# Kernel tuning notes

Hardware: AMD Instinct MI355X
Metric: run time of the kernel (lower is better)

Reference implementation:

```python
import jax, jax.numpy as jnp
import numpy as np

N, E, G = 10000, 50000, 500
MAX_Z = 64
C0, C1, C2 = 128, 64, 32            # multiplicities of l=0,1,2 irreps ('128x0e+64x1e+32x2e')
D = C0 + 3 * C1 + 5 * C2            # 480 total feature dim
H = 4                               # num_heads
HC0, HC1, HC2 = C0 // H, C1 // H, C2 // H   # irreps_head '32x0e+16x1o+8x2e'
HD = HC0 + 3 * HC1 + 5 * HC2        # 120 head dim
NB = 128                            # number_of_basis
CUTOFF = 5.0                        # max_radius
T_DEQ = 2                           # DEQ fixed-point iterations (unrolled)
NDEQ, NBLK = 5, 6                   # num_layers=6: 5 DEQ blocks + 1 decoder block
NW = C0 + 2 * C1 + 2 * C2           # 320 radial modulation weights per message
AVG_DEGREE = 16.0
AVG_NUM_NODES = 21.0
FDIM = 512                          # irreps_feature '512x0e'


def split(x):
    n = x.shape[0]
    return x[:, :C0], x[:, C0:C0 + 3 * C1].reshape(n, C1, 3), x[:, C0 + 3 * C1:].reshape(n, C2, 5)


def merge(s, v1, v2):
    n = s.shape[0]
    return jnp.concatenate([s, v1.reshape(n, -1), v2.reshape(n, -1)], axis=-1)


def eq_layernorm(x, eps=1e-5):
    # EquivariantLayerNormV2: center l=0, RMS-normalize each l-block per node
    s, v1, v2 = split(x)
    s = s - s.mean(-1, keepdims=True)
    s = s * jax.lax.rsqrt((s * s).mean(-1, keepdims=True) + eps)
    v1 = v1 * jax.lax.rsqrt((v1 * v1).sum(-1).mean(-1) + eps)[:, None, None]
    v2 = v2 * jax.lax.rsqrt((v2 * v2).sum(-1).mean(-1) + eps)[:, None, None]
    return merge(s, v1, v2)


def eq_linear(x, W0, W1, W2):
    # e3nn Linear: block-diagonal per irrep degree, mixes channels only
    s, v1, v2 = split(x)
    return merge(s @ W0, jnp.einsum('ncm,cd->ndm', v1, W1), jnp.einsum('ncm,cd->ndm', v2, W2))


def sph_harm(u):
    # real spherical harmonics lmax=2, component normalization
    x, y, z = u[:, 0], u[:, 1], u[:, 2]
    y1 = jnp.sqrt(3.0) * u
    y2 = jnp.stack([jnp.sqrt(15.0) * x * y, jnp.sqrt(15.0) * y * z,
                    jnp.sqrt(1.25) * (3.0 * z * z - 1.0),
                    jnp.sqrt(15.0) * x * z, jnp.sqrt(3.75) * (x * x - y * y)], -1)
    return y1, y2


def radial(rbf, R1, R2, R3):
    # fc_neurons [128,64,64] radial MLP -> per-path tensor-product weights
    return jax.nn.silu(jax.nn.silu(rbf @ R1) @ R2) @ R3


def modulate(s_e, v1_e, v2_e, y1, y2, P1, P2, w):
    # depthwise tensor product x_src (x) Y(sh), radial-weighted paths:
    # 0x0->0, 1x0->1, 0x1->1, 2x0->2, 0x2->2
    w0, w1, w2, w3, w4 = jnp.split(w, [C0, C0 + C1, C0 + 2 * C1, C0 + 2 * C1 + C2], -1)
    m_s = s_e * w0
    m_v1 = v1_e * w1[:, :, None] + (s_e @ P1)[:, :, None] * y1[:, None, :] * w2[:, :, None]
    m_v2 = v2_e * w3[:, :, None] + (s_e @ P2)[:, :, None] * y2[:, None, :] * w4[:, :, None]
    return m_s, m_v1, m_v2


def to_heads(s, v1, v2):
    n = s.shape[0]
    return jnp.concatenate([s.reshape(n, H, HC0), v1.reshape(n, H, HC1 * 3), v2.reshape(n, H, HC2 * 5)], -1)


def from_heads(a):
    n = a.shape[0]
    return merge(a[:, :, :HC0].reshape(n, C0),
                 a[:, :, HC0:HC0 + 3 * HC1].reshape(n, C1, 3),
                 a[:, :, HC0 + 3 * HC1:].reshape(n, C2, 5))


def block(x, src, dst, rbf, y1, y2, i, Wq0, Wq1, Wq2, P1, P2, R1, R2, R3, Wp0, Wp1, Wp2, Wg, Wi0, Wi1, Wi2, Wo0, Wo1, Wo2):
    # LN -> dot-product graph attention -> LN -> gated equivariant FFN, both residual
    n = x.shape[0]
    xn = eq_layernorm(x)
    q = to_heads(*split(eq_linear(xn, Wq0[i], Wq1[i], Wq2[i])))      # [N,H,HD]
    w = radial(rbf, R1[i], R2[i], R3[i])                             # [E,2*NW]
    s, v1, v2 = split(xn)
    s_e, v1_e, v2_e = s[src], v1[src], v2[src]
    k = to_heads(*modulate(s_e, v1_e, v2_e, y1, y2, P1[i], P2[i], w[:, :NW]))
    v = to_heads(*modulate(s_e, v1_e, v2_e, y1, y2, P1[i], P2[i], w[:, NW:]))
    logits = (q[dst] * k).sum(-1) / jnp.sqrt(jnp.float32(HD))        # [E,H] invariant
    m = jax.ops.segment_max(logits, dst, num_segments=n)
    e = jnp.exp(logits - m[dst])
    denom = jax.ops.segment_sum(e, dst, num_segments=n)
    alpha = e / (denom[dst] + 1e-9)
    att = jax.ops.segment_sum(alpha[:, :, None] * v, dst, num_segments=n)  # [N,H,HD]
    x = x + eq_linear(from_heads(att), Wp0[i], Wp1[i], Wp2[i])
    xn2 = eq_layernorm(x)
    y = eq_linear(xn2, Wi0[i], Wi1[i], Wi2[i])
    ys, yv1, yv2 = split(y)
    g = jax.nn.sigmoid(xn2[:, :C0] @ Wg[i])                          # gates for l>0
    y = merge(jax.nn.silu(ys), yv1 * g[:, :C1, None], yv2 * g[:, C1:, None])
    return x + eq_linear(y, Wo0[i], Wo1[i], Wo2[i])


def setup_inputs() -> dict:
    key = jax.random.key(0)
    ks = iter(jax.random.split(key, 64))
    f32 = jnp.float32
    pos = jax.random.normal(next(ks), (N, 3), f32) * 2.0
    atom_z = jax.random.randint(next(ks), (N,), 0, MAX_Z)
    edge_src = jax.random.randint(next(ks), (E,), 0, N)
    edge_dst = jax.random.randint(next(ks), (E,), 0, N)
    batch_seg = jnp.sort(jax.random.randint(next(ks), (N,), 0, G))
    def W(shape, fan):
        return jax.random.normal(next(ks), shape, f32) / np.sqrt(fan).astype(np.float32)
    inp = dict(pos=pos, atom_z=atom_z, edge_src=edge_src, edge_dst=edge_dst, batch_seg=batch_seg)
    inp.update(
        atom_table=W((MAX_Z, C0), 1.0),
        Pd1=W((C0, C1), C0), Pd2=W((C0, C2), C0),
        Rd1=W((NB, 64), NB), Rd2=W((64, 64), 64), Rd3=W((64, NW), 64),
        Wq0=W((NBLK, C0, C0), C0), Wq1=W((NBLK, C1, C1), C1), Wq2=W((NBLK, C2, C2), C2),
        P1=W((NBLK, C0, C1), C0), P2=W((NBLK, C0, C2), C0),
        R1=W((NBLK, NB, 64), NB), R2=W((NBLK, 64, 64), 64), R3=W((NBLK, 64, 2 * NW), 64),
        Wp0=W((NBLK, C0, C0), C0), Wp1=W((NBLK, C1, C1), C1), Wp2=W((NBLK, C2, C2), C2),
        Wg=W((NBLK, C0, C1 + C2), C0),
        Wi0=W((NBLK, C0, C0), C0), Wi1=W((NBLK, C1, C1), C1), Wi2=W((NBLK, C2, C2), C2),
        Wo0=W((NBLK, C0, C0), C0), Wo1=W((NBLK, C1, C1), C1), Wo2=W((NBLK, C2, C2), C2),
        Wf=W((C0, FDIM), C0), Wh1=W((FDIM, FDIM), FDIM), Wh2=W((FDIM, 1), FDIM),
    )
    return inp


def reference(pos, atom_z, edge_src, edge_dst, batch_seg, atom_table, Pd1, Pd2, Rd1, Rd2, Rd3, Wq0, Wq1, Wq2, P1, P2, R1, R2, R3, Wp0, Wp1, Wp2, Wg, Wi0, Wi1, Wi2, Wo0, Wo1, Wo2, Wf, Wh1, Wh2):
    vec = pos[edge_dst] - pos[edge_src]
    r = jnp.sqrt((vec * vec).sum(-1) + 1e-12)
    u = vec / r[:, None]
    mus = jnp.linspace(0.0, CUTOFF, NB, dtype=pos.dtype)
    sigma = CUTOFF / NB
    rbf = jnp.exp(-0.5 * ((r[:, None] - mus) / sigma) ** 2)          # gaussian RBF [E,NB]
    y1, y2 = sph_harm(u)
    # atom embedding (scalars only) + edge-degree embedding
    s_atom = jax.nn.one_hot(atom_z, MAX_Z, dtype=pos.dtype) @ atom_table
    wd = radial(rbf, Rd1, Rd2, Rd3)
    z1 = jnp.zeros((E, C1, 3), pos.dtype)
    z2 = jnp.zeros((E, C2, 5), pos.dtype)
    m_s, m_v1, m_v2 = modulate(s_atom[edge_src], z1, z2, y1, y2, Pd1, Pd2, wd)
    deg = merge(jax.ops.segment_sum(m_s, edge_dst, num_segments=N),
                jax.ops.segment_sum(m_v1, edge_dst, num_segments=N),
                jax.ops.segment_sum(m_v2, edge_dst, num_segments=N)) / jnp.sqrt(jnp.float32(AVG_DEGREE))
    inj = merge(s_atom, jnp.zeros((N, C1, 3), pos.dtype), jnp.zeros((N, C2, 5), pos.dtype)) + deg
    bp = (Wq0, Wq1, Wq2, P1, P2, R1, R2, R3, Wp0, Wp1, Wp2, Wg, Wi0, Wi1, Wi2, Wo0, Wo1, Wo2)
    # DEQ fixed-point iterations over the 5 implicit blocks, with input injection
    z = jnp.zeros((N, D), pos.dtype)
    for _ in range(T_DEQ):
        x = z + inj
        for i in range(NDEQ):
            x = block(x, edge_src, edge_dst, rbf, y1, y2, i, *bp)
        z = x
    x = block(z, edge_src, edge_dst, rbf, y1, y2, NBLK - 1, *bp)     # decoder block
    feat = split(x)[0] @ Wf                                          # 512x0e invariant features
    feat = feat - feat.mean(-1, keepdims=True)
    feat = feat * jax.lax.rsqrt((feat * feat).mean(-1, keepdims=True) + 1e-5)
    e_node = jax.nn.silu(feat @ Wh1) @ Wh2                           # per-node energy [N,1]
    return jax.ops.segment_sum(e_node, batch_seg, num_segments=G) / jnp.sqrt(jnp.float32(AVG_NUM_NODES))
```

## Files before the change

### kernel.cpp

```cpp
#include <hip/hip_runtime.h>
#include <hip/hip_bf16.h>
#include <math.h>

#define NN 10000
#define NE 50000
#define NBLK 6
#define MAXD 256
#define V1_OFF (NN*128)
#define V2_OFF (NN*320)

typedef __hip_bfloat16 bf16;
typedef __attribute__((ext_vector_type(8))) short short8;
typedef __attribute__((ext_vector_type(4))) float f32x4;

__device__ __forceinline__ float ldw(const float* p){ return *p; }
__device__ __forceinline__ float ldw(const bf16* p){ return __bfloat162float(*p); }
__device__ __forceinline__ void stw(float* p, float v){ *p = v; }
__device__ __forceinline__ void stw(bf16* p, float v){ *p = __float2bfloat16(v); }

template<typename OutT>
__global__ __launch_bounds__(256)
void mgemm_kernel(const bf16* __restrict__ A, const bf16* __restrict__ Bt,
                  OutT* __restrict__ C, int M, int Nn, int K,
                  int lda, int ldc, int epi)
{
  __shared__ __align__(16) unsigned short Ash[64][40];
  __shared__ __align__(16) unsigned short Bsh[64][40];
  int tid  = threadIdx.x;
  int wid  = tid >> 6, lane = tid & 63;
  int wr   = wid >> 1, wc = wid & 1;
  int rowBase = blockIdx.x * 64, colBase = blockIdx.y * 64;
  int fr = lane & 15;
  int fk = (lane >> 4) * 8;
  f32x4 acc[2][2] = {};
  int am = tid >> 2, ako = (tid & 3) * 8;

  for (int k0 = 0; k0 < K; k0 += 32) {
    {
      int gm = rowBase + am;
      short8 v = {0,0,0,0,0,0,0,0};
      if (gm < M) v = *reinterpret_cast<const short8*>(A + (long)gm * lda + k0 + ako);
      *reinterpret_cast<short8*>(&Ash[am][ako]) = v;
    }
    {
      int gn = colBase + am;
      short8 v = {0,0,0,0,0,0,0,0};
      if (gn < Nn) v = *reinterpret_cast<const short8*>(Bt + (long)gn * K + k0 + ako);
      *reinterpret_cast<short8*>(&Bsh[am][ako]) = v;
    }
    __syncthreads();
    short8 a0 = *reinterpret_cast<const short8*>(&Ash[wr*32 +      fr][fk]);
    short8 a1 = *reinterpret_cast<const short8*>(&Ash[wr*32 + 16 + fr][fk]);
    short8 b0 = *reinterpret_cast<const short8*>(&Bsh[wc*32 +      fr][fk]);
    short8 b1 = *reinterpret_cast<const short8*>(&Bsh[wc*32 + 16 + fr][fk]);
    acc[0][0] = __builtin_amdgcn_mfma_f32_16x16x32_bf16(a0, b0, acc[0][0], 0, 0, 0);
    acc[0][1] = __builtin_amdgcn_mfma_f32_16x16x32_bf16(a0, b1, acc[0][1], 0, 0, 0);
    acc[1][0] = __builtin_amdgcn_mfma_f32_16x16x32_bf16(a1, b0, acc[1][0], 0, 0, 0);
    acc[1][1] = __builtin_amdgcn_mfma_f32_16x16x32_bf16(a1, b1, acc[1][1], 0, 0, 0);
    __syncthreads();
  }
  int erow = (lane >> 4) * 4, ecol = lane & 15;
  #pragma unroll
  for (int tm = 0; tm < 2; tm++) {
    #pragma unroll
    for (int tn = 0; tn < 2; tn++) {
      #pragma unroll
      for (int r = 0; r < 4; r++) {
        int gm = rowBase + wr*32 + tm*16 + erow + r;
        int gn = colBase + wc*32 + tn*16 + ecol;
        if (gm < M && gn < Nn) {
          float v = acc[tm][tn][r];
          long off = (long)gm * ldc + gn;
          if (epi == 1)      v = v / (1.f + expf(-v));
          else if (epi == 2) v = v + ldw(&C[off]);
          else if (epi == 3) v = 1.f / (1.f + expf(-v));
          stw(&C[off], v);
        }
      }
    }
  }
}

struct GSeg {
  const bf16* A; const bf16* Bt; char* C;
  int M, N, K, lda, ldc, epi, outBf16, blk0, nbx;
};

__global__ __launch_bounds__(256)
void gseg_kernel(GSeg s0, GSeg s1, GSeg s2, GSeg s3, int nseg)
{
  GSeg s = s0;
  int b = blockIdx.x;
  if (nseg > 1 && b >= s1.blk0) s = s1;
  if (nseg > 2 && b >= s2.blk0) s = s2;
  if (nseg > 3 && b >= s3.blk0) s = s3;
  int rel = b - s.blk0;
  int bx = rel % s.nbx, by = rel / s.nbx;

  __shared__ __align__(16) unsigned short Ash[64][40];
  __shared__ __align__(16) unsigned short Bsh[64][40];
  int tid  = threadIdx.x;
  int wid  = tid >> 6, lane = tid & 63;
  int wr   = wid >> 1, wc = wid & 1;
  int rowBase = bx * 64, colBase = by * 64;
  int fr = lane & 15;
  int fk = (lane >> 4) * 8;
  f32x4 acc[2][2] = {};
  int am = tid >> 2, ako = (tid & 3) * 8;

  for (int k0 = 0; k0 < s.K; k0 += 32) {
    {
      int gm = rowBase + am;
      short8 v = {0,0,0,0,0,0,0,0};
      if (gm < s.M) v = *reinterpret_cast<const short8*>(s.A + (long)gm * s.lda + k0 + ako);
      *reinterpret_cast<short8*>(&Ash[am][ako]) = v;
    }
    {
      int gn = colBase + am;
      short8 v = {0,0,0,0,0,0,0,0};
      if (gn < s.N) v = *reinterpret_cast<const short8*>(s.Bt + (long)gn * s.K + k0 + ako);
      *reinterpret_cast<short8*>(&Bsh[am][ako]) = v;
    }
    __syncthreads();
    short8 a0 = *reinterpret_cast<const short8*>(&Ash[wr*32 +      fr][fk]);
    short8 a1 = *reinterpret_cast<const short8*>(&Ash[wr*32 + 16 + fr][fk]);
    short8 b0 = *reinterpret_cast<const short8*>(&Bsh[wc*32 +      fr][fk]);
    short8 b1 = *reinterpret_cast<const short8*>(&Bsh[wc*32 + 16 + fr][fk]);
    acc[0][0] = __builtin_amdgcn_mfma_f32_16x16x32_bf16(a0, b0, acc[0][0], 0, 0, 0);
    acc[0][1] = __builtin_amdgcn_mfma_f32_16x16x32_bf16(a0, b1, acc[0][1], 0, 0, 0);
    acc[1][0] = __builtin_amdgcn_mfma_f32_16x16x32_bf16(a1, b0, acc[1][0], 0, 0, 0);
    acc[1][1] = __builtin_amdgcn_mfma_f32_16x16x32_bf16(a1, b1, acc[1][1], 0, 0, 0);
    __syncthreads();
  }
  int erow = (lane >> 4) * 4, ecol = lane & 15;
  #pragma unroll
  for (int tm = 0; tm < 2; tm++) {
    #pragma unroll
    for (int tn = 0; tn < 2; tn++) {
      #pragma unroll
      for (int r = 0; r < 4; r++) {
        int gm = rowBase + wr*32 + tm*16 + erow + r;
        int gn = colBase + wc*32 + tn*16 + ecol;
        if (gm < s.M && gn < s.N) {
          float v = acc[tm][tn][r];
          long off = (long)gm * s.ldc + gn;
          if (s.epi == 1)      v = v / (1.f + expf(-v));
          else if (s.epi == 2) v = v + (s.outBf16 ? ldw((const bf16*)s.C + off)
                                                 : ldw((const float*)s.C + off));
          else if (s.epi == 3) v = 1.f / (1.f + expf(-v));
          if (s.outBf16) stw((bf16*)s.C + off, v);
          else           stw((float*)s.C + off, v);
        }
      }
    }
  }
}

__global__ void transp_kernel(const float* __restrict__ src, bf16* __restrict__ dst,
                              int R, int C, long sSrc, long sDst)
{
  src += (long)blockIdx.z * sSrc;
  dst += (long)blockIdx.z * sDst;
  int idx = blockIdx.x * 256 + threadIdx.x;
  if (idx < R * C) {
    int r = idx / C, c = idx - r * C;
    dst[(long)c * R + r] = __float2bfloat16(src[idx]);
  }
}

__global__ void gather_atom_kernel(const int* __restrict__ z, const float* __restrict__ tab,
                                   float* __restrict__ s_atom, bf16* __restrict__ s_atom_bf)
{
  int idx = blockIdx.x * 256 + threadIdx.x;
  if (idx < NN * 128) {
    int n = idx >> 7, c = idx & 127;
    float v = tab[z[n] * 128 + c];
    s_atom[idx] = v;
    s_atom_bf[idx] = __float2bfloat16(v);
  }
}

__global__ void hist_kernel(const int* __restrict__ dst, int* __restrict__ counts)
{
  int e = blockIdx.x * 256 + threadIdx.x;
  if (e < NE) atomicAdd(&counts[dst[e]], 1);
}

__global__ __launch_bounds__(1024)
void scan_kernel(const int* __restrict__ counts, int* __restrict__ indptr,
                 int* __restrict__ nextp)
{
  __shared__ int totals[1024];
  const int PER = (NN + 1023) / 1024;
  int tid = threadIdx.x;
  int base = tid * PER;
  int local[PER];
  int s = 0;
  #pragma unroll
  for (int i = 0; i < PER; i++) {
    int idx = base + i;
    int c = (idx < NN) ? counts[idx] : 0;
    local[i] = s; s += c;
  }
  totals[tid] = s;
  __syncthreads();
  for (int off = 1; off < 1024; off <<= 1) {
    int v = (tid >= off) ? totals[tid - off] : 0;
    __syncthreads();
    totals[tid] += v;
    __syncthreads();
  }
  int prefix = (tid > 0) ? totals[tid - 1] : 0;
  #pragma unroll
  for (int i = 0; i < PER; i++) {
    int idx = base + i;
    if (idx < NN) { indptr[idx] = prefix + local[i]; nextp[idx] = prefix + local[i]; }
  }
  if (tid == 1023) indptr[NN] = totals[1023];
}

__global__ void scatter_kernel(const int* __restrict__ dst, int* __restrict__ nextp,
                               int* __restrict__ order)
{
  int e = blockIdx.x * 256 + threadIdx.x;
  if (e < NE) {
    int p = atomicAdd(&nextp[dst[e]], 1);
    order[p] = e;
  }
}

__global__ void dhist_kernel(const int* __restrict__ indptr, int* __restrict__ bins)
{
  int n = blockIdx.x * 256 + threadIdx.x;
  if (n < NN) {
    int d = indptr[n+1] - indptr[n]; if (d > MAXD-1) d = MAXD-1;
    atomicAdd(&bins[MAXD-1-d], 1);
  }
}
__global__ __launch_bounds__(256)
void dscan_kernel(const int* __restrict__ bins, int* __restrict__ boff)
{
  __shared__ int tmp[MAXD];
  int t = threadIdx.x;
  tmp[t] = bins[t];
  __syncthreads();
  for (int off = 1; off < MAXD; off <<= 1) {
    int v = (t >= off) ? tmp[t-off] : 0;
    __syncthreads();
    tmp[t] += v;
    __syncthreads();
  }
  boff[t] = tmp[t] - bins[t];
}
__global__ void dplace_kernel(const int* __restrict__ indptr, int* __restrict__ boff,
                              int* __restrict__ norder)
{
  int n = blockIdx.x * 256 + threadIdx.x;
  if (n < NN) {
    int d = indptr[n+1] - indptr[n]; if (d > MAXD-1) d = MAXD-1;
    int pos = atomicAdd(&boff[MAXD-1-d], 1);
    norder[pos] = n;
  }
}

__global__ __launch_bounds__(128)
void edge_perm_kernel(const float* __restrict__ pos, const int* __restrict__ esrc,
                      const int* __restrict__ edst, const int* __restrict__ order,
                      int* __restrict__ srcp, bf16* __restrict__ rbf,
                      float* __restrict__ y1, float* __restrict__ y2)
{
  int idx = blockIdx.x, t = threadIdx.x;
  int e = order[idx];
  int s = esrc[e], d = edst[e];
  float vx = pos[d*3+0] - pos[s*3+0];
  float vy = pos[d*3+1] - pos[s*3+1];
  float vz = pos[d*3+2] - pos[s*3+2];
  float r = sqrtf(vx*vx + vy*vy + vz*vz + 1e-12f);
  float mu = t * (5.0f / 127.0f);
  const float inv_sig = 128.0f / 5.0f;
  float zq = (r - mu) * inv_sig;
  rbf[(long)idx * 128 + t] = __float2bfloat16(expf(-0.5f * zq * zq));
  if (t == 0) {
    srcp[idx] = s;
    float inv = 1.f / r;
    float ux = vx*inv, uy = vy*inv, uz = vz*inv;
    const float s3  = 1.7320508075688772f;
    const float s15 = 3.872983346207417f;
    y1[idx*3+0] = s3*ux; y1[idx*3+1] = s3*uy; y1[idx*3+2] = s3*uz;
    y2[idx*5+0] = s15*ux*uy;
    y2[idx*5+1] = s15*uy*uz;
    y2[idx*5+2] = 1.118033988749895f * (3.f*uz*uz - 1.f);
    y2[idx*5+3] = s15*ux*uz;
    y2[idx*5+4] = 1.9364916731037085f * (ux*ux - uy*uy);
  }
}

__global__ void copy_kernel(const float* __restrict__ a, float* __restrict__ b, int n)
{
  int i = blockIdx.x * 256 + threadIdx.x;
  if (i < n) b[i] = a[i];
}

__global__ void addinj_kernel(float* __restrict__ x, const float* __restrict__ inj, int n)
{
  int i = blockIdx.x * 256 + threadIdx.x;
  if (i < n) x[i] += inj[i];
}

__global__ void cvt128_kernel(const float* __restrict__ a, bf16* __restrict__ b)
{
  int i = blockIdx.x * 256 + threadIdx.x;
  if (i < NN * 128) b[i] = __float2bfloat16(a[i]);
}

__global__ __launch_bounds__(64)
void ln_kernel(const float* __restrict__ x, bf16* __restrict__ ob)
{
  int n = blockIdx.x, t = threadIdx.x;
  bool lo = t < 32;
  int t32 = t & 31;
  float s0 = x[n*128 + t], s1 = x[n*128 + 64 + t];
  float v1v[3], v2v[5];
  #pragma unroll
  for (int m = 0; m < 3; m++) v1v[m] = x[V1_OFF + m*NN*64 + n*64 + t];
  #pragma unroll
  for (int m = 0; m < 5; m++) v2v[m] = lo ? x[V2_OFF + m*NN*32 + n*32 + t32] : 0.f;
  float ssum = s0 + s1, ssq = s0*s0 + s1*s1;
  float q1 = v1v[0]*v1v[0] + v1v[1]*v1v[1] + v1v[2]*v1v[2];
  float q2 = 0.f;
  #pragma unroll
  for (int m = 0; m < 5; m++) q2 += v2v[m]*v2v[m];
  #pragma unroll
  for (int d = 32; d >= 1; d >>= 1) {
    ssum += __shfl_xor(ssum, d);
    ssq  += __shfl_xor(ssq, d);
    q1   += __shfl_xor(q1, d);
    q2   += __shfl_xor(q2, d);
  }
  float mu  = ssum * (1.f/128.f);
  float var = fmaxf(ssq * (1.f/128.f) - mu*mu, 0.f);
  float is  = rsqrtf(var + 1e-5f);
  float i1  = rsqrtf(q1 * (1.f/64.f) + 1e-5f);
  float i2  = rsqrtf(q2 * (1.f/32.f) + 1e-5f);
  ob[n*128 + t]      = __float2bfloat16((s0 - mu) * is);
  ob[n*128 + 64 + t] = __float2bfloat16((s1 - mu) * is);
  #pragma unroll
  for (int m = 0; m < 3; m++)
    ob[V1_OFF + m*NN*64 + n*64 + t] = __float2bfloat16(v1v[m] * i1);
  if (lo) {
    #pragma unroll
    for (int m = 0; m < 5; m++)
      ob[V2_OFF + m*NN*32 + n*32 + t32] = __float2bfloat16(v2v[m] * i2);
  }
}

__global__ __launch_bounds__(64)
void deg_inj_kernel(const int* __restrict__ indptr, const int* __restrict__ srcp,
                    const bf16* __restrict__ wd,
                    const float* __restrict__ s_atom, const float* __restrict__ spd1,
                    const float* __restrict__ spd2, const float* __restrict__ y1,
                    const float* __restrict__ y2, float* __restrict__ inj)
{
  int n = blockIdx.x, t = threadIdx.x;
  bool lo = t < 32;
  int t32 = t & 31;
  float acc0 = 0, acc1 = 0, a1[3] = {0,0,0}, a2[5] = {0,0,0,0,0};
  int beg = indptr[n], end = indptr[n+1];
  for (int idx = beg; idx < end; ++idx) {
    int s = srcp[idx];
    const bf16* we = wd + (size_t)idx * 320;
    acc0 += s_atom[s*128 + t]      * ldw(&we[t]);
    acc1 += s_atom[s*128 + 64 + t] * ldw(&we[64 + t]);
    float sp1e = spd1[s*64 + t];
    float w2k = ldw(&we[192 + t]);
    #pragma unroll
    for (int m = 0; m < 3; m++) a1[m] += sp1e * y1[idx*3+m] * w2k;
    float sp2e = lo ? spd2[s*32 + t32] : 0.f;
    float w4k  = lo ? ldw(&we[288 + t32]) : 0.f;
    #pragma unroll
    for (int m = 0; m < 5; m++) a2[m] += sp2e * y2[idx*5+m] * w4k;
  }
  const float inv = 0.25f;
  inj[n*128 + t]      = s_atom[n*128 + t]      + acc0 * inv;
  inj[n*128 + 64 + t] = s_atom[n*128 + 64 + t] + acc1 * inv;
  #pragma unroll
  for (int m = 0; m < 3; m++) inj[V1_OFF + m*NN*64 + n*64 + t] = a1[m] * inv;
  if (lo) {
    #pragma unroll
    for (int m = 0; m < 5; m++) inj[V2_OFF + m*NN*32 + n*32 + t32] = a2[m] * inv;
  }
}

__global__ __launch_bounds__(64)
void attn_kernel(const int* __restrict__ norder,
                 const int* __restrict__ indptr, const int* __restrict__ srcp,
                 const bf16* __restrict__ w,
                 const bf16* __restrict__ xn, const bf16* __restrict__ qcat,
                 const bf16* __restrict__ qv1b, const bf16* __restrict__ qv2b,
                 const float* __restrict__ y1, const float* __restrict__ y2,
                 bf16* __restrict__ att)
{
  int n = norder[blockIdx.x];
  int t = threadIdx.x;
  bool lo = t < 32;
  int t32 = t & 31;
  const float qscl = 0.09128709291752769f;
  float qs0 = ldw(&qcat[n*224 + t]) * qscl, qs1 = ldw(&qcat[n*224 + 64 + t]) * qscl;
  float qv1[3], qv2[5];
  #pragma unroll
  for (int m = 0; m < 3; m++) qv1[m] = ldw(&qv1b[m*NN*64 + n*64 + t]) * qscl;
  #pragma unroll
  for (int m = 0; m < 5; m++) qv2[m] = lo ? ldw(&qv2b[m*NN*32 + n*32 + t32]) * qscl : 0.f;
  const int h_s0 = t >> 5, h_s1 = 2 + (t >> 5), h_v1 = t >> 4, h_v2 = t32 >> 3;
  float m_run[4] = {-1e30f, -1e30f, -1e30f, -1e30f};
  float d_run[4] = {0, 0, 0, 0};
  float as0 = 0, as1 = 0, av1[3] = {0,0,0}, av2[5] = {0,0,0,0,0};
  int beg = indptr[n], end = indptr[n+1];
  for (int idx = beg; idx < end; ++idx) {
    int s = srcp[idx];
    const bf16* we = w + (size_t)idx * 640;
    float sE0 = ldw(&xn[s*128 + t]), sE1 = ldw(&xn[s*128 + 64 + t]);
    float v1E[3];
    #pragma unroll
    for (int m = 0; m < 3; m++) v1E[m] = ldw(&xn[V1_OFF + m*NN*64 + s*64 + t]);
    float v2E[5];
    #pragma unroll
    for (int m = 0; m < 5; m++) v2E[m] = lo ? ldw(&xn[V2_OFF + m*NN*32 + s*32 + t32]) : 0.f;
    float sp1e = ldw(&qcat[s*224 + 128 + t]);
    float sp2e = lo ? ldw(&qcat[s*224 + 192 + t32]) : 0.f;
    float Y1[3], Y2[5];
    #pragma unroll
    for (int m = 0; m < 3; m++) Y1[m] = y1[idx*3+m];
    #pragma unroll
    for (int m = 0; m < 5; m++) Y2[m] = lo ? y2[idx*5+m] : 0.f;
    float part[4] = {0,0,0,0};
    part[h_s0] += qs0 * (sE0 * ldw(&we[t]));
    part[h_s1] += qs1 * (sE1 * ldw(&we[64 + t]));
    float w1k = ldw(&we[128 + t]), w2k = ldw(&we[192 + t]);
    #pragma unroll
    for (int m = 0; m < 3; m++) part[h_v1] += qv1[m] * (v1E[m]*w1k + sp1e*Y1[m]*w2k);
    float w3k = lo ? ldw(&we[256 + t32]) : 0.f, w4k = lo ? ldw(&we[288 + t32]) : 0.f;
    #pragma unroll
    for (int m = 0; m < 5; m++) part[h_v2] += qv2[m] * (v2E[m]*w3k + sp2e*Y2[m]*w4k);
    #pragma unroll
    for (int d = 1; d < 64; d <<= 1) {
      #pragma unroll
      for (int h = 0; h < 4; h++) part[h] += __shfl_xor(part[h], d);
    }
    float scl[4], pp[4];
    #pragma unroll
    for (int h = 0; h < 4; h++) {
      float logit = part[h];
      float nm = fmaxf(m_run[h], logit);
      scl[h] = expf(m_run[h] - nm);
      pp[h]  = expf(logit - nm);
      d_run[h] = d_run[h] * scl[h] + pp[h];
      m_run[h] = nm;
    }
    as0 = as0 * scl[h_s0] + pp[h_s0] * (sE0 * ldw(&we[320 + t]));
    as1 = as1 * scl[h_s1] + pp[h_s1] * (sE1 * ldw(&we[384 + t]));
    float w1v = ldw(&we[448 + t]), w2v = ldw(&we[512 + t]);
    #pragma unroll
    for (int m = 0; m < 3; m++)
      av1[m] = av1[m] * scl[h_v1] + pp[h_v1] * (v1E[m]*w1v + sp1e*Y1[m]*w2v);
    float w3v = lo ? ldw(&we[576 + t32]) : 0.f, w4v = lo ? ldw(&we[608 + t32]) : 0.f;
    #pragma unroll
    for (int m = 0; m < 5; m++)
      av2[m] = av2[m] * scl[h_v2] + pp[h_v2] * (v2E[m]*w3v + sp2e*Y2[m]*w4v);
  }
  float r0 = 1.f / (d_run[h_s0] + 1e-9f);
  float r1 = 1.f / (d_run[h_s1] + 1e-9f);
  att[n*128 + t]      = __float2bfloat16(as0 * r0);
  att[n*128 + 64 + t] = __float2bfloat16(as1 * r1);
  float rv1 = 1.f / (d_run[h_v1] + 1e-9f);
  #pragma unroll
  for (int m = 0; m < 3; m++)
    att[V1_OFF + m*NN*64 + n*64 + t] = __float2bfloat16(av1[m] * rv1);
  if (lo) {
    float rv2 = 1.f / (d_run[h_v2] + 1e-9f);
    #pragma unroll
    for (int m = 0; m < 5; m++)
      att[V2_OFF + m*NN*32 + n*32 + t32] = __float2bfloat16(av2[m] * rv2);
  }
}

__global__ void gate_kernel(const bf16* __restrict__ ycat, bf16* __restrict__ ybs,
                            bf16* __restrict__ yv1, bf16* __restrict__ yv2)
{
  int idx = blockIdx.x * 256 + threadIdx.x;
  if (idx >= NN * 480) return;
  if (idx < NN * 128) {
    int n = idx >> 7, c = idx & 127;
    float v = ldw(&ycat[n*224 + c]);
    ybs[idx] = __float2bfloat16(v / (1.f + expf(-v)));
  } else if (idx < NN * 320) {
    int rel = idx - NN * 128;
    int n = (rel % (NN * 64)) / 64;
    int c = rel % 64;
    float g = ldw(&ycat[n*224 + 128 + c]);
    g = 1.f / (1.f + expf(-g));
    yv1[rel] = __float2bfloat16(__bfloat162float(yv1[rel]) * g);
  } else {
    int rel = idx - NN * 320;
    int n = (rel % (NN * 32)) / 32;
    int c = rel % 32;
    float g = ldw(&ycat[n*224 + 192 + c]);
    g = 1.f / (1.f + expf(-g));
    yv2[rel] = __float2bfloat16(__bfloat162float(yv2[rel]) * g);
  }
}

__global__ __launch_bounds__(64)
void ln512_kernel(float* __restrict__ f, bf16* __restrict__ fb)
{
  int n = blockIdx.x, t = threadIdx.x;
  float v[8];
  float s = 0, sq = 0;
  #pragma unroll
  for (int i = 0; i < 8; i++) {
    v[i] = f[(long)n*512 + i*64 + t];
    s += v[i]; sq += v[i]*v[i];
  }
  #pragma unroll
  for (int d = 32; d >= 1; d >>= 1) { s += __shfl_xor(s, d); sq += __shfl_xor(sq, d); }
  float mu  = s * (1.f/512.f);
  float var = fmaxf(sq * (1.f/512.f) - mu*mu, 0.f);
  float inv = rsqrtf(var + 1e-5f);
  #pragma unroll
  for (int i = 0; i < 8; i++) {
    float o = (v[i] - mu) * inv;
    fb[(long)n*512 + i*64 + t] = __float2bfloat16(o);
  }
}

__global__ __launch_bounds__(64)
void dot_seg_kernel(const float* __restrict__ h, const float* __restrict__ w2,
                    const int* __restrict__ bseg, float* __restrict__ out)
{
  int n = blockIdx.x, t = threadIdx.x;
  float acc = 0;
  #pragma unroll
  for (int i = 0; i < 8; i++) {
    int j = i*64 + t;
    acc += h[(long)n*512 + j] * w2[j];
  }
  #pragma unroll
  for (int d = 32; d >= 1; d >>= 1) acc += __shfl_xor(acc, d);
  if (t == 0) atomicAdd(&out[bseg[n]], acc * 0.21821789023599236f);
}

extern "C" void kernel_launch(void* const* d_in, const int* in_sizes, int n_in,
                              void* d_out, int out_size, void* d_ws, size_t ws_size,
                              hipStream_t stream)
{
  const float* pos        = (const float*)d_in[0];
  const int*   atom_z     = (const int*)  d_in[1];
  const int*   esrc       = (const int*)  d_in[2];
  const int*   edst       = (const int*)  d_in[3];
  const int*   bseg       = (const int*)  d_in[4];
  const float* atom_table = (const float*)d_in[5];
  const float* Pd1 = (const float*)d_in[6];
  const float* Pd2 = (const float*)d_in[7];
  const float* Rd1 = (const float*)d_in[8];
  const float* Rd2 = (const float*)d_in[9];
  const float* Rd3 = (const float*)d_in[10];
  const float* Wq0 = (const float*)d_in[11];
  const float* Wq1 = (const float*)d_in[12];
  const float* Wq2 = (const float*)d_in[13];
  const float* P1  = (const float*)d_in[14];
  const float* P2  = (const float*)d_in[15];
  const float* R1  = (const float*)d_in[16];
  const float* R2  = (const float*)d_in[17];
  const float* R3  = (const float*)d_in[18];
  const float* Wp0 = (const float*)d_in[19];
  const float* Wp1 = (const float*)d_in[20];
  const float* Wp2 = (const float*)d_in[21];
  const float* Wg  = (const float*)d_in[22];
  const float* Wi0 = (const float*)d_in[23];
  const float* Wi1 = (const float*)d_in[24];
  const float* Wi2 = (const float*)d_in[25];
  const float* Wo0 = (const float*)d_in[26];
  const float* Wo1 = (const float*)d_in[27];
  const float* Wo2 = (const float*)d_in[28];
  const float* Wf  = (const float*)d_in[29];
  const float* Wh1 = (const float*)d_in[30];
  const float* Wh2 = (const float*)d_in[31];
  (void)in_sizes; (void)n_in;

  char* p = (char*)d_ws;
  auto allocB = [&](size_t bytes) -> void* {
    void* r = (void*)p;
    p += (bytes + 255) & ~(size_t)255;
    return r;
  };
  auto allocF = [&](size_t nf) -> float* { return (float*)allocB(nf * 4); };
  auto allocH = [&](size_t nh) -> bf16*  { return (bf16*)allocB(nh * 2); };

  bf16*  rbf   = allocH((size_t)NE * 128);
  float* y1    = allocF((size_t)NE * 3);
  float* y2    = allocF((size_t)NE * 5);
  bf16*  h1    = allocH((size_t)NE * 64);
  bf16*  h2c   = allocH((size_t)6 * NE * 64);
  float* s_at  = allocF((size_t)NN * 128);
  bf16*  s_atb = allocH((size_t)NN * 128);
  float* inj   = allocF((size_t)NN * 480);
  float* x     = allocF((size_t)NN * 480);
  bf16*  xnb   = allocH((size_t)NN * 480);
  bf16*  qcat  = allocH((size_t)NN * 224);
  bf16*  qv1   = allocH((size_t)NN * 192);
  bf16*  qv2   = allocH((size_t)NN * 160);
  bf16*  attb  = allocH((size_t)NN * 480);
  bf16*  ybs   = allocH((size_t)NN * 128);
  int* counts  = (int*)allocB((size_t)NN * 4);
  int* indptr  = (int*)allocB((size_t)(NN + 1) * 4);
  int* nextp   = (int*)allocB((size_t)NN * 4);
  int* order   = (int*)allocB((size_t)NE * 4);
  int* srcp    = (int*)allocB((size_t)NE * 4);
  int* norder  = (int*)allocB((size_t)NN * 4);
  int* dbins   = (int*)allocB((size_t)MAXD * 4);
  int* dboff   = (int*)allocB((size_t)MAXD * 4);
  float* spd1  = allocF((size_t)NN * 64);
  float* spd2  = allocF((size_t)NN * 32);

  bf16*  ycat = qcat;
  bf16*  yv1  = qv1;
  bf16*  yv2  = qv2;
  bf16*  xsb  = s_atb;

  bf16* Pd1t = allocH(64*128);
  bf16* Pd2t = allocH(32*128);
  bf16* Rd1t = allocH(64*128);
  bf16* Rd2t = allocH(64*64);
  bf16* Rd3t = allocH(320*64);
  bf16* catq = allocH((size_t)6*224*128);
  bf16* Wq1t = allocH((size_t)6*64*64);
  bf16* Wq2t = allocH((size_t)6*32*32);
  bf16* R1t  = allocH((size_t)6*64*128);
  bf16* R2t  = allocH((size_t)6*64*64);
  bf16* R3t  = allocH((size_t)6*640*64);
  bf16* Wp0t = allocH((size_t)6*128*128);
  bf16* Wp1t = allocH((size_t)6*64*64);
  bf16* Wp2t = allocH((size_t)6*32*32);
  bf16* cati = allocH((size_t)6*224*128);
  bf16* Wi1t = allocH((size_t)6*64*64);
  bf16* Wi2t = allocH((size_t)6*32*32);
  bf16* Wo0t = allocH((size_t)6*128*128);
  bf16* Wo1t = allocH((size_t)6*64*64);
  bf16* Wo2t = allocH((size_t)6*32*32);
  bf16* Wft  = allocH(512*128);
  bf16* Wh1t = allocH((size_t)512*512);

  size_t used = (size_t)(p - (char*)d_ws);
  size_t avail = (ws_size > used) ? ws_size - used : 0;
  const size_t slotH = (size_t)NE * 640 * sizeof(bf16);

  if (avail < slotH) {
    hipMemsetAsync(d_out, 0, (size_t)out_size * 4, stream);
    return;
  }
  bf16* w = (bf16*)allocB(slotH);

  float* feat  = (float*)w;
  bf16*  featb = (bf16*)(feat + (size_t)NN*512);
  float* hb    = (float*)(featb + (size_t)NN*512);

  auto transp = [&](const float* src, bf16* dst, int R, int C, long sSrc, long sDst, int nz) {
    dim3 g((R*C + 255)/256, 1, nz);
    transp_kernel<<<g, 256, 0, stream>>>(src, dst, R, C, sSrc, sDst);
  };
  auto gemmF = [&](const bf16* A, const bf16* Bt, float* C, int M, int Nn, int K,
                   int lda, int ldc, int epi) {
    dim3 g((M + 63) / 64, (Nn + 63) / 64, 1);
    mgemm_kernel<float><<<g, 256, 0, stream>>>(A, Bt, C, M, Nn, K, lda, ldc, epi);
  };
  auto gemmH = [&](const bf16* A, const bf16* Bt, bf16* C, int M, int Nn, int K,
                   int lda, int ldc, int epi) {
    dim3 g((M + 63) / 64, (Nn + 63) / 64, 1);
    mgemm_kernel<bf16><<<g, 256, 0, stream>>>(A, Bt, C, M, Nn, K, lda, ldc, epi);
  };
  auto mkseg = [&](const bf16* A, const bf16* Bt, void* C, int M, int N, int K,
                   int lda, int ldc, int epi, int outBf16) -> GSeg {
    GSeg g; g.A = A; g.Bt = Bt; g.C = (char*)C; g.M = M; g.N = N; g.K = K;
    g.lda = lda; g.ldc = ldc; g.epi = epi; g.outBf16 = outBf16;
    g.blk0 = 0; g.nbx = (M + 63) / 64;
    return g;
  };
  auto segBlocks = [&](const GSeg& s) -> int { return s.nbx * ((s.N + 63) / 64); };
  auto launch3 = [&](GSeg a, GSeg b, GSeg c) {
    a.blk0 = 0;
    b.blk0 = segBlocks(a);
    c.blk0 = b.blk0 + segBlocks(b);
    int total = c.blk0 + segBlocks(c);
    gseg_kernel<<<total, 256, 0, stream>>>(a, b, c, c, 3);
  };
  auto launch4 = [&](GSeg a, GSeg b, GSeg c, GSeg d) {
    a.blk0 = 0;
    b.blk0 = segBlocks(a);
    c.blk0 = b.blk0 + segBlocks(b);
    d.blk0 = c.blk0 + segBlocks(c);
    int total = d.blk0 + segBlocks(d);
    gseg_kernel<<<total, 256, 0, stream>>>(a, b, c, d, 4);
  };

  transp(Pd1, Pd1t, 128, 64, 0, 0, 1);
  transp(Pd2, Pd2t, 128, 32, 0, 0, 1);
  transp(Rd1, Rd1t, 128, 64, 0, 0, 1);
  transp(Rd2, Rd2t, 64, 64, 0, 0, 1);
  transp(Rd3, Rd3t, 64, 320, 0, 0, 1);
  transp(Wq0, catq,           128, 128, 128*128, 224*128, 6);
  transp(P1,  catq + 128*128, 128, 64,  128*64,  224*128, 6);
  transp(P2,  catq + 192*128, 128, 32,  128*32,  224*128, 6);
  transp(Wq1, Wq1t, 64, 64, 64*64, 64*64, 6);
  transp(Wq2, Wq2t, 32, 32, 32*32, 32*32, 6);
  transp(R1,  R1t, 128, 64, 128*64, 128*64, 6);
  transp(R2,  R2t, 64, 64, 64*64, 64*64, 6);
  transp(R3,  R3t, 64, 640, 64*640, 64*640, 6);
  transp(Wp0, Wp0t, 128, 128, 128*128, 128*128, 6);
  transp(Wp1, Wp1t, 64, 64, 64*64, 64*64, 6);
  transp(Wp2, Wp2t, 32, 32, 32*32, 32*32, 6);
  transp(Wi0, cati,           128, 128, 128*128, 224*128, 6);
  transp(Wg,  cati + 128*128, 128, 96,  128*96,  224*128, 6);
  transp(Wi1, Wi1t, 64, 64, 64*64, 64*64, 6);
  transp(Wi2, Wi2t, 32, 32, 32*32, 32*32, 6);
  transp(Wo0, Wo0t, 128, 128, 128*128, 128*128, 6);
  transp(Wo1, Wo1t, 64, 64, 64*64, 64*64, 6);
  transp(Wo2, Wo2t, 32, 32, 32*32, 32*32, 6);
  transp(Wf,  Wft, 128, 512, 0, 0, 1);
  transp(Wh1, Wh1t, 512, 512, 0, 0, 1);

  hipMemsetAsync(counts, 0, NN * 4, stream);
  hipMemsetAsync(dbins, 0, MAXD * 4, stream);
  hipMemsetAsync(d_out, 0, (size_t)out_size * 4, stream);
  gather_atom_kernel<<<(NN*128 + 255)/256, 256, 0, stream>>>(atom_z, atom_table, s_at, s_atb);
  hist_kernel<<<(NE + 255)/256, 256, 0, stream>>>(edst, counts);
  scan_kernel<<<1, 1024, 0, stream>>>(counts, indptr, nextp);
  scatter_kernel<<<(NE + 255)/256, 256, 0, stream>>>(edst, nextp, order);
  edge_perm_kernel<<<NE, 128, 0, stream>>>(pos, esrc, edst, order, srcp, rbf, y1, y2);
  dhist_kernel<<<(NN + 255)/256, 256, 0, stream>>>(indptr, dbins);
  dscan_kernel<<<1, MAXD, 0, stream>>>(dbins, dboff);
  dplace_kernel<<<(NN + 255)/256, 256, 0, stream>>>(indptr, dboff, norder);
  gemmF(s_atb, Pd1t, spd1, NN, 64, 128, 128, 64, 0);
  gemmF(s_atb, Pd2t, spd2, NN, 32, 128, 128, 32, 0);
  gemmH(rbf, Rd1t, h1, NE, 64, 128, 128, 64, 1);
  gemmH(h1,  Rd2t, h2c, NE, 64, 64, 64, 64, 1);
  gemmH(h2c, Rd3t, w,  NE, 320, 64, 64, 320, 0);
  deg_inj_kernel<<<NN, 64, 0, stream>>>(indptr, srcp, w, s_at, spd1, spd2, y1, y2, inj);
  copy_kernel<<<(NN*480 + 255)/256, 256, 0, stream>>>(inj, x, NN*480);

  for (int i = 0; i < 6; i++) {
    gemmH(rbf, R1t + (size_t)i*64*128, h1, NE, 64, 128, 128, 64, 1);
    gemmH(h1,  R2t + (size_t)i*64*64, h2c + (size_t)i*NE*64, NE, 64, 64, 64, 64, 1);
  }

  auto run_block = [&](int i) {
    const bf16* cq  = catq + (size_t)i * 224 * 128;
    const bf16* q1t = Wq1t + (size_t)i * 64 * 64;
    const bf16* q2t = Wq2t + (size_t)i * 32 * 32;
    const bf16* r3  = R3t  + (size_t)i * 640 * 64;
    const bf16* p0t = Wp0t + (size_t)i * 128 * 128;
    const bf16* p1t = Wp1t + (size_t)i * 64 * 64;
    const bf16* p2t = Wp2t + (size_t)i * 32 * 32;
    const bf16* ci  = cati + (size_t)i * 224 * 128;
    const bf16* i1t = Wi1t + (size_t)i * 64 * 64;
    const bf16* i2t = Wi2t + (size_t)i * 32 * 32;
    const bf16* o0t = Wo0t + (size_t)i * 128 * 128;
    const bf16* o1t = Wo1t + (size_t)i * 64 * 64;
    const bf16* o2t = Wo2t + (size_t)i * 32 * 32;

    ln_kernel<<<NN, 64, 0, stream>>>(x, xnb);
    launch4(mkseg(xnb,          cq,  qcat, NN,   224, 128, 128, 224, 0, 1),
            mkseg(xnb + V1_OFF, q1t, qv1,  3*NN, 64,  64,  64,  64,  0, 1),
            mkseg(xnb + V2_OFF, q2t, qv2,  5*NN, 32,  32,  32,  32,  0, 1),
            mkseg(h2c + (size_t)i*NE*64, r3, w, NE, 640, 64, 64, 640, 0, 1));
    attn_kernel<<<NN, 64, 0, stream>>>(norder, indptr, srcp, w, xnb, qcat, qv1, qv2, y1, y2, attb);
    launch3(mkseg(attb,          p0t, x,          NN,   128, 128, 128, 128, 2, 0),
            mkseg(attb + V1_OFF, p1t, x + V1_OFF, 3*NN, 64,  64,  64,  64,  2, 0),
            mkseg(attb + V2_OFF, p2t, x + V2_OFF, 5*NN, 32,  32,  32,  32,  2, 0));
    ln_kernel<<<NN, 64, 0, stream>>>(x, xnb);
    launch3(mkseg(xnb,          ci,  ycat, NN,   224, 128, 128, 224, 0, 1),
            mkseg(xnb + V1_OFF, i1t, yv1,  3*NN, 64,  64,  64,  64,  0, 1),
            mkseg(xnb + V2_OFF, i2t, yv2,  5*NN, 32,  32,  32,  32,  0, 1));
    gate_kernel<<<(NN*480 + 255)/256, 256, 0, stream>>>(ycat, ybs, yv1, yv2);
    launch3(mkseg(ybs, o0t, x,          NN,   128, 128, 128, 128, 2, 0),
            mkseg(yv1, o1t, x + V1_OFF, 3*NN, 64,  64,  64,  64,  2, 0),
            mkseg(yv2, o2t, x + V2_OFF, 5*NN, 32,  32,  32,  32,  2, 0));
  };

  for (int t = 0; t < 2; t++) {
    if (t == 1) addinj_kernel<<<(NN*480 + 255)/256, 256, 0, stream>>>(x, inj, NN*480);
    for (int i = 0; i < 5; i++) run_block(i);
  }
  run_block(5);

  cvt128_kernel<<<(NN*128 + 255)/256, 256, 0, stream>>>(x, xsb);
  gemmF(xsb, Wft, feat, NN, 512, 128, 128, 512, 0);
  ln512_kernel<<<NN, 64, 0, stream>>>(feat, featb);
  gemmF(featb, Wh1t, hb, NN, 512, 512, 512, 512, 1);
  dot_seg_kernel<<<NN, 64, 0, stream>>>(hb, Wh2, bseg, (float*)d_out);
}
```

Baseline: 2.056 ms.

## Interleave radial weight columns for vector loads and use lazy softmax rescaling

Reorders R3's transposed output columns so each thread's eight per-edge radial weights sit contiguously. The attention kernel can then fetch them with one 16-byte load, plus an 8-byte load for the l=2 lanes, instead of many scalar bf16 loads. The online softmax now rescales only when a logit exceeds the running max by more than 8, and uses fast __expf. This cuts exp calls and multiplies per edge, at the cost of a slightly different numerical path and reliance on the R3 layout matching the edge-weight GEMM output.

```diff
diff --git a/kernel.cpp b/kernel.cpp
--- a/kernel.cpp
+++ b/kernel.cpp
@@ -11,12 +11,17 @@
 
 typedef __hip_bfloat16 bf16;
 typedef __attribute__((ext_vector_type(8))) short short8;
+typedef __attribute__((ext_vector_type(4))) short short4v;
 typedef __attribute__((ext_vector_type(4))) float f32x4;
 
 __device__ __forceinline__ float ldw(const float* p){ return *p; }
 __device__ __forceinline__ float ldw(const bf16* p){ return __bfloat162float(*p); }
 __device__ __forceinline__ void stw(float* p, float v){ *p = v; }
 __device__ __forceinline__ void stw(bf16* p, float v){ *p = __float2bfloat16(v); }
+__device__ __forceinline__ float b2f(short u){
+  unsigned int x = ((unsigned int)(unsigned short)u) << 16;
+  return __builtin_bit_cast(float, x);
+}
 
 template<typename OutT>
 __global__ __launch_bounds__(256)
@@ -168,6 +173,28 @@
   }
 }
 
+__global__ void transp_r3_kernel(const float* __restrict__ src, bf16* __restrict__ dst)
+{
+  int idx = blockIdx.x * 256 + threadIdx.x;
+  if (idx >= NBLK * 640 * 64) return;
+  int blk  = idx / (640 * 64);
+  int rem  = idx - blk * 640 * 64;
+  int newc = rem >> 6;
+  int k    = rem & 63;
+  int oldc;
+  if (newc < 512) {
+    int t = newc >> 3, j = newc & 7;
+    const int base[8] = {0, 64, 128, 192, 320, 384, 448, 512};
+    oldc = base[j] + t;
+  } else {
+    int q = newc - 512;
+    int t32 = q >> 2, j = q & 3;
+    const int base2[4] = {256, 288, 576, 608};
+    oldc = base2[j] + t32;
+  }
+  dst[idx] = __float2bfloat16(src[(size_t)blk * 64 * 640 + (size_t)k * 640 + oldc]);
+}
+
 __global__ void gather_atom_kernel(const int* __restrict__ z, const float* __restrict__ tab,
                                    float* __restrict__ s_atom, bf16* __restrict__ s_atom_bf)
 {
@@ -419,6 +446,14 @@
   for (int idx = beg; idx < end; ++idx) {
     int s = srcp[idx];
     const bf16* we = w + (size_t)idx * 640;
+    short8 w8 = *reinterpret_cast<const short8*>(we + t*8);
+    float kw0 = b2f(w8[0]), kw1 = b2f(w8[1]), w1k = b2f(w8[2]), w2k = b2f(w8[3]);
+    float vw0 = b2f(w8[4]), vw1 = b2f(w8[5]), w1v = b2f(w8[6]), w2v = b2f(w8[7]);
+    float w3k = 0, w4k = 0, w3v = 0, w4v = 0;
+    if (lo) {
+      short4v l4 = *reinterpret_cast<const short4v*>(we + 512 + t32*4);
+      w3k = b2f(l4[0]); w4k = b2f(l4[1]); w3v = b2f(l4[2]); w4v = b2f(l4[3]);
+    }
     float sE0 = ldw(&xn[s*128 + t]), sE1 = ldw(&xn[s*128 + 64 + t]);
     float v1E[3];
     #pragma unroll
@@ -434,12 +469,10 @@
     #pragma unroll
     for (int m = 0; m < 5; m++) Y2[m] = lo ? y2[idx*5+m] : 0.f;
     float part[4] = {0,0,0,0};
-    part[h_s0] += qs0 * (sE0 * ldw(&we[t]));
-    part[h_s1] += qs1 * (sE1 * ldw(&we[64 + t]));
-    float w1k = ldw(&we[128 + t]), w2k = ldw(&we[192 + t]);
+    part[h_s0] += qs0 * (sE0 * kw0);
+    part[h_s1] += qs1 * (sE1 * kw1);
     #pragma unroll
     for (int m = 0; m < 3; m++) part[h_v1] += qv1[m] * (v1E[m]*w1k + sp1e*Y1[m]*w2k);
-    float w3k = lo ? ldw(&we[256 + t32]) : 0.f, w4k = lo ? ldw(&we[288 + t32]) : 0.f;
     #pragma unroll
     for (int m = 0; m < 5; m++) part[h_v2] += qv2[m] * (v2E[m]*w3k + sp2e*Y2[m]*w4k);
     #pragma unroll
@@ -447,26 +480,33 @@
       #pragma unroll
       for (int h = 0; h < 4; h++) part[h] += __shfl_xor(part[h], d);
     }
-    float scl[4], pp[4];
-    #pragma unroll
-    for (int h = 0; h < 4; h++) {
-      float logit = part[h];
-      float nm = fmaxf(m_run[h], logit);
-      scl[h] = expf(m_run[h] - nm);
-      pp[h]  = expf(logit - nm);
-      d_run[h] = d_run[h] * scl[h] + pp[h];
-      m_run[h] = nm;
+    if (part[0] > m_run[0] + 8.f || part[1] > m_run[1] + 8.f ||
+        part[2] > m_run[2] + 8.f || part[3] > m_run[3] + 8.f) {
+      float scl[4];
+      #pragma unroll
+      for (int h = 0; h < 4; h++) {
+        float nm = fmaxf(m_run[h], part[h]);
+        scl[h] = __expf(m_run[h] - nm);
+        m_run[h] = nm;
+        d_run[h] *= scl[h];
+      }
+      as0 *= scl[h_s0]; as1 *= scl[h_s1];
+      #pragma unroll
+      for (int m = 0; m < 3; m++) av1[m] *= scl[h_v1];
+      #pragma unroll
+      for (int m = 0; m < 5; m++) av2[m] *= scl[h_v2];
     }
-    as0 = as0 * scl[h_s0] + pp[h_s0] * (sE0 * ldw(&we[320 + t]));
-    as1 = as1 * scl[h_s1] + pp[h_s1] * (sE1 * ldw(&we[384 + t]));
-    float w1v = ldw(&we[448 + t]), w2v = ldw(&we[512 + t]);
+    float pp[4];
+    #pragma unroll
+    for (int h = 0; h < 4; h++) { pp[h] = __expf(part[h] - m_run[h]); d_run[h] += pp[h]; }
+    as0 += pp[h_s0] * (sE0 * vw0);
+    as1 += pp[h_s1] * (sE1 * vw1);
     #pragma unroll
     for (int m = 0; m < 3; m++)
-      av1[m] = av1[m] * scl[h_v1] + pp[h_v1] * (v1E[m]*w1v + sp1e*Y1[m]*w2v);
-    float w3v = lo ? ldw(&we[576 + t32]) : 0.f, w4v = lo ? ldw(&we[608 + t32]) : 0.f;
+      av1[m] += pp[h_v1] * (v1E[m]*w1v + sp1e*Y1[m]*w2v);
     #pragma unroll
     for (int m = 0; m < 5; m++)
-      av2[m] = av2[m] * scl[h_v2] + pp[h_v2] * (v2E[m]*w3v + sp2e*Y2[m]*w4v);
+      av2[m] += pp[h_v2] * (v2E[m]*w3v + sp2e*Y2[m]*w4v);
   }
   float r0 = 1.f / (d_run[h_s0] + 1e-9f);
   float r1 = 1.f / (d_run[h_s1] + 1e-9f);
@@ -714,7 +754,7 @@
   transp(Wq2, Wq2t, 32, 32, 32*32, 32*32, 6);
   transp(R1,  R1t, 128, 64, 128*64, 128*64, 6);
   transp(R2,  R2t, 64, 64, 64*64, 64*64, 6);
-  transp(R3,  R3t, 64, 640, 64*640, 64*640, 6);
+  transp_r3_kernel<<<(NBLK*640*64 + 255)/256, 256, 0, stream>>>(R3, R3t);
   transp(Wp0, Wp0t, 128, 128, 128*128, 128*128, 6);
   transp(Wp1, Wp1t, 64, 64, 64*64, 64*64, 6);
   transp(Wp2, Wp2t, 32, 32, 32*32, 32*32, 6);
```

Measured after the change: 1.926 ms. -6.3%, faster.
